# Kernel optimization log

Hardware: AMD Instinct MI355X
Metric: run time of the kernel (lower is better)

Reference implementation:

```python
import jax, jax.numpy as jnp
import numpy as np
from jax import lax

NS, W, BS, NSENT, EMB, H, NMEN, NCAND, NTOK, NENTV = 640, 64, 16, 40, 512, 256, 32, 32, 50000, 100000


def _gru_dir(xp, valid, Whh, bhh):
    # xp: [T,B,3H] precomputed input projection; valid: [T,B] bool
    h0 = jnp.zeros((xp.shape[1], Whh.shape[1]), xp.dtype)
    def step(h, inp):
        x, v = inp
        g = h @ Whh.T + bhh
        xr, xz, xn = jnp.split(x, 3, axis=-1)
        hr, hz, hn = jnp.split(g, 3, axis=-1)
        r = jax.nn.sigmoid(xr + hr)
        z = jax.nn.sigmoid(xz + hz)
        n = jnp.tanh(xn + r * hn)
        hnew = (1.0 - z) * n + z * h
        hnew = jnp.where(v[:, None], hnew, h)  # freeze state past seq end (packed-seq semantics)
        return hnew, hnew * v[:, None]         # zero padded outputs like pad_packed_sequence
    _, ys = lax.scan(step, h0, (xp, valid))
    return ys  # [T,B,H]


def _att_birnn(x, lens, Wih_f, Whh_f, bih_f, bhh_f, Wih_b, Whh_b, bih_b, bhh_b, lin_w, lin_b, attw):
    # x: [B,T,I], lens: [B] (descending, lens[0]==T) -> attended pooling [B,2H]
    T = x.shape[1]
    valid = jnp.arange(T)[:, None] < lens[None, :]  # [T,B]
    xp_f = jnp.einsum('bti,oi->tbo', x, Wih_f) + bih_f
    xp_b = jnp.einsum('bti,oi->tbo', x, Wih_b) + bih_b
    ys_f = _gru_dir(xp_f, valid, Whh_f, bhh_f)
    ys_b = _gru_dir(xp_b[::-1], valid[::-1], Whh_b, bhh_b)[::-1]
    enc = jnp.concatenate([ys_f, ys_b], -1)  # [T,B,2H]
    emb_h = jnp.tanh(jnp.einsum('tbh,oh->tbo', enc, lin_w) + lin_b)
    att = emb_h @ attw  # [T,B]
    e = jnp.exp(att) * valid  # original uses raw exp with additive 1e-4 denom
    wgt = e / (jnp.sum(e, 0, keepdims=True) + 1e-4)
    return jnp.sum(wgt[..., None] * enc, 0)  # [B,2H]


def _cos(a, b, eps=1e-8):
    dot = jnp.sum(a * b, -1)
    na = jnp.sqrt(jnp.sum(a * a, -1))
    nb = jnp.sqrt(jnp.sum(b * b, -1))
    return dot / jnp.maximum(na * nb, eps)


def _forward(batch_doc, sent_order, length_sent, length_doc, men_sent_idx, can_ent_idx, cand_mask,
             embed_doc, embed_ent, wp, sp, mlp_w, mlp_b):
    emb_w = embed_doc[batch_doc]                         # [NS,W,EMB]; eval mode -> no dropout
    sent_embs = _att_birnn(emb_w, length_sent, *wp)      # [NS,2H]
    padded = jnp.concatenate([jnp.zeros((1, sent_embs.shape[1]), sent_embs.dtype), sent_embs], 0)
    each_sent = padded[sent_order]                       # [BS,NSENT,2H] (_reorder_sent)
    doc_embs = _att_birnn(each_sent, length_doc, *sp)    # [BS,2H]
    emb_ent = embed_ent[can_ent_idx]                     # [BS,NMEN,NCAND,EMB]
    sent_vecs = each_sent[jnp.arange(each_sent.shape[0])[:, None], men_sent_idx]  # [BS,NMEN,2H]
    # vectorized replacement of the triple python loop of per-element cosine sims
    ss = _cos(sent_vecs[:, :, None, :], emb_ent) * cand_mask  # [BS,NMEN,NCAND]
    ds = _cos(doc_embs[:, None, None, :], emb_ent) * cand_mask
    cc = jnp.concatenate([ss, ds], -1)                   # [BS,NMEN,2*NCAND]
    mask = (ss != 0).astype(cc.dtype)
    return (cc @ mlp_w.T + mlp_b) * mask


def setup_inputs() -> dict:
    key = jax.random.key(0)
    ks = jax.random.split(key, 36)
    batch_doc = jax.random.randint(ks[0], (NS, W), 0, NTOK, dtype=jnp.int32)
    length_sent = jnp.sort(jax.random.randint(ks[1], (NS,), 1, W + 1, dtype=jnp.int32))[::-1].at[0].set(W)
    length_doc = jnp.sort(jax.random.randint(ks[2], (BS,), 1, NSENT + 1, dtype=jnp.int32))[::-1].at[0].set(NSENT)
    so = jax.random.randint(ks[3], (BS, NSENT), 1, NS + 1, dtype=jnp.int32)
    sent_order = jnp.where(jnp.arange(NSENT)[None, :] < length_doc[:, None], so, 0)
    men_sent_idx = jax.random.randint(ks[4], (BS, NMEN), 0, NSENT, dtype=jnp.int32) % length_doc[:, None]
    can_ent_idx = jax.random.randint(ks[5], (BS, NMEN, NCAND), 1, NENTV, dtype=jnp.int32)
    cand_mask = (jax.random.uniform(ks[6], (BS, NMEN, NCAND)) < 0.8).astype(jnp.float32)
    def nrm(k, shape, s=0.05):
        return s * jax.random.normal(k, shape, dtype=jnp.float32)
    embed_doc = nrm(ks[7], (NTOK, EMB)).at[0].set(0.0)   # padding_idx=0
    embed_ent = nrm(ks[8], (NENTV, EMB)).at[0].set(0.0)
    d = {
        'batch_doc': batch_doc, 'sent_order': sent_order, 'length_sent': length_sent,
        'length_doc': length_doc, 'men_sent_idx': men_sent_idx, 'can_ent_idx': can_ent_idx,
        'cand_mask': cand_mask, 'embed_doc': embed_doc, 'embed_ent': embed_ent,
        'w_Wih_f': nrm(ks[9], (3 * H, EMB)), 'w_Whh_f': nrm(ks[10], (3 * H, H)),
        'w_bih_f': nrm(ks[11], (3 * H,)), 'w_bhh_f': nrm(ks[12], (3 * H,)),
        'w_Wih_b': nrm(ks[13], (3 * H, EMB)), 'w_Whh_b': nrm(ks[14], (3 * H, H)),
        'w_bih_b': nrm(ks[15], (3 * H,)), 'w_bhh_b': nrm(ks[16], (3 * H,)),
        'w_lin_w': nrm(ks[17], (2 * H, 2 * H)), 'w_lin_b': nrm(ks[18], (2 * H,)),
        'w_attw': nrm(ks[19], (2 * H,)),
        's_Wih_f': nrm(ks[20], (3 * H, 2 * H)), 's_Whh_f': nrm(ks[21], (3 * H, H)),
        's_bih_f': nrm(ks[22], (3 * H,)), 's_bhh_f': nrm(ks[23], (3 * H,)),
        's_Wih_b': nrm(ks[24], (3 * H, 2 * H)), 's_Whh_b': nrm(ks[25], (3 * H, H)),
        's_bih_b': nrm(ks[26], (3 * H,)), 's_bhh_b': nrm(ks[27], (3 * H,)),
        's_lin_w': nrm(ks[28], (2 * H, 2 * H)), 's_lin_b': nrm(ks[29], (2 * H,)),
        's_attw': nrm(ks[30], (2 * H,)),
        'mlp_w': nrm(ks[31], (NCAND, 2 * NCAND)), 'mlp_b': nrm(ks[32], (NCAND,)),
    }
    return d


def reference(batch_doc, sent_order, length_sent, length_doc, men_sent_idx, can_ent_idx, cand_mask,
              embed_doc, embed_ent,
              w_Wih_f, w_Whh_f, w_bih_f, w_bhh_f, w_Wih_b, w_Whh_b, w_bih_b, w_bhh_b, w_lin_w, w_lin_b, w_attw,
              s_Wih_f, s_Whh_f, s_bih_f, s_bhh_f, s_Wih_b, s_Whh_b, s_bih_b, s_bhh_b, s_lin_w, s_lin_b, s_attw,
              mlp_w, mlp_b):
    wp = (w_Wih_f, w_Whh_f, w_bih_f, w_bhh_f, w_Wih_b, w_Whh_b, w_bih_b, w_bhh_b, w_lin_w, w_lin_b, w_attw)
    sp = (s_Wih_f, s_Whh_f, s_bih_f, s_bhh_f, s_Wih_b, s_Whh_b, s_bih_b, s_bhh_b, s_lin_w, s_lin_b, s_attw)
    return _forward(batch_doc, sent_order, length_sent, length_doc, men_sent_idx, can_ent_idx, cand_mask,
                    embed_doc, embed_ent, wp, sp, mlp_w, mlp_b)
```

## Files before the change

kernel.cpp:

```cpp
#include <hip/hip_runtime.h>
#include <cstdint>
#include <cstddef>


typedef __attribute__((ext_vector_type(8))) short bf16x8;
typedef __attribute__((ext_vector_type(4))) float f32x4;

__device__ __forceinline__ float bfraw2f(unsigned int u16) {
    unsigned int x = u16 << 16; float f; __builtin_memcpy(&f, &x, 4); return f;
}
__device__ __forceinline__ unsigned short f2bfraw(float f) {
    unsigned int u; __builtin_memcpy(&u, &f, 4);
    unsigned int r = u + 0x7fffu + ((u >> 16) & 1u);
    return (unsigned short)(r >> 16);
}
__device__ __forceinline__ unsigned short f2h(float f) {
    _Float16 h = (_Float16)f; unsigned short u; __builtin_memcpy(&u, &h, 2); return u;
}
__device__ __forceinline__ float h2f(unsigned short u) {
    _Float16 h; __builtin_memcpy(&h, &u, 2); return (float)h;
}
__device__ __forceinline__ float bflo(unsigned int p) {
    unsigned int x = p << 16; float f; __builtin_memcpy(&f, &x, 4); return f;
}
__device__ __forceinline__ float bfhi(unsigned int p) {
    unsigned int x = p & 0xffff0000u; float f; __builtin_memcpy(&f, &x, 4); return f;
}
__device__ __forceinline__ float fast_sigmoid(float x) { return 1.f / (1.f + __expf(-x)); }
__device__ __forceinline__ float fast_tanh(float x) {
    x = fminf(fmaxf(x, -30.f), 30.f);
    float e = __expf(2.f * x);
    return (e - 1.f) / (e + 1.f);
}
__device__ __forceinline__ float fin(float x) {
    return (x == x && fabsf(x) < 1e30f) ? x : 0.f;
}

__device__ __forceinline__ float ldsc(const void* p, size_t i, int m) {
    return m ? bfraw2f(((const unsigned short*)p)[i]) : ((const float*)p)[i];
}
__device__ __forceinline__ bf16x8 ld8bf(const void* p, size_t ei, int m) {
    if (m) return *(const bf16x8*)((const unsigned short*)p + ei);
    const float* f = (const float*)p + ei;
    f32x4 a = *(const f32x4*)f, b = *(const f32x4*)(f + 4);
    bf16x8 r;
    r[0] = (short)f2bfraw(a[0]); r[1] = (short)f2bfraw(a[1]);
    r[2] = (short)f2bfraw(a[2]); r[3] = (short)f2bfraw(a[3]);
    r[4] = (short)f2bfraw(b[0]); r[5] = (short)f2bfraw(b[1]);
    r[6] = (short)f2bfraw(b[2]); r[7] = (short)f2bfraw(b[3]);
    return r;
}
__device__ __forceinline__ void ld8f(const void* p, size_t ei, int m, float* o) {
    if (m) {
        uint4 wv = *(const uint4*)((const unsigned short*)p + ei);
        o[0] = bflo(wv.x); o[1] = bfhi(wv.x); o[2] = bflo(wv.y); o[3] = bfhi(wv.y);
        o[4] = bflo(wv.z); o[5] = bfhi(wv.z); o[6] = bflo(wv.w); o[7] = bfhi(wv.w);
    } else {
        const float* f = (const float*)p + ei;
        #pragma unroll
        for (int i = 0; i < 8; ++i) o[i] = f[i];
    }
}

__global__ void k_probe(const unsigned short* __restrict__ w, int* __restrict__ flag) {
    if (threadIdx.x == 0) {
        int bad = 0;
        for (int i = 0; i < 512; ++i) {
            float v = bfraw2f(w[i]);
            if (!(fabsf(v) <= 1.0f)) bad++;
        }
        flag[0] = (bad == 0) ? 1 : 0;
        flag[1] = 1;
    }
}

__global__ void p_cvt(const void* __restrict__ src, unsigned short* __restrict__ dst,
                      int n, const int* __restrict__ modep) {
    const int m = modep[0];
    for (int i = blockIdx.x * 256 + threadIdx.x; i < n; i += gridDim.x * 256)
        dst[i] = f2bfraw(ldsc(src, i, m));
}

__global__ void p_whh_swz(const void* __restrict__ whh, unsigned short* __restrict__ dst,
                          const int* __restrict__ modep) {
    const int m = modep[0];
    const int idx = blockIdx.x * 256 + threadIdx.x;
    if (idx >= 24576) return;
    const int lane = idx & 63, ks = (idx >> 6) & 7;
    const int g = (idx >> 9) % 6, w = idx / 3072;
    const int lm = lane & 15, q = lane >> 4;
    const int reg = g >> 1, nt = g & 1;
    const int row = reg * 256 + w * 32 + nt * 16 + lm;
    const size_t src = (size_t)row * 256 + ks * 32 + q * 8;
    const size_t d = (size_t)idx * 8;
    #pragma unroll
    for (int e = 0; e < 8; ++e) dst[d + e] = f2bfraw(ldsc(whh, src + e, m));
}

__global__ __launch_bounds__(256, 2) void k_xp_word(
    const void* __restrict__ embA, const int* __restrict__ batch_doc,
    const unsigned short* __restrict__ wih,
    const void* __restrict__ bih_f, const void* __restrict__ bih_b,
    unsigned short* __restrict__ xp, int b0, int nb,
    const int* __restrict__ amode, const int* __restrict__ modep)
{
    __shared__ unsigned short As[64][40];
    __shared__ unsigned short Bs[256][40];
    const int am = amode[0], m = modep[0];
    const int bm = blockIdx.x, bc = blockIdx.y;
    const int tid = threadIdx.x;
    const int wave = tid >> 6, lane = tid & 63, lm = lane & 15, q = lane >> 4;
    const int arow = tid >> 2, akoff = (tid & 3) * 8;
    const int r = bm * 64 + arow;
    const int tt = r / nb, bl = r - tt * nb;
    const size_t aei = (size_t)batch_doc[(b0 + bl) * 64 + tt] * 512 + akoff;

    const f32x4 fzero = {0.f, 0.f, 0.f, 0.f};
    f32x4 acc[4][4];
    #pragma unroll
    for (int i = 0; i < 4; ++i)
        #pragma unroll
        for (int j = 0; j < 4; ++j) acc[i][j] = fzero;

    for (int kt = 0; kt < 16; ++kt) {
        *(bf16x8*)&As[arow][akoff] = ld8bf(embA, aei + kt * 32, am);
        #pragma unroll
        for (int ld = 0; ld < 4; ++ld) {
            int e = ld * 256 + tid;
            int n = e >> 2, koff = (e & 3) * 8;
            int gn = bc * 256 + n;
            *(uint4*)&Bs[n][koff] = *(const uint4*)(wih + (size_t)gn * 512 + kt * 32 + koff);
        }
        __syncthreads();
        bf16x8 af[4], bv[4];
        #pragma unroll
        for (int mt = 0; mt < 4; ++mt) af[mt] = *(const bf16x8*)&As[mt * 16 + lm][q * 8];
        #pragma unroll
        for (int nt = 0; nt < 4; ++nt) bv[nt] = *(const bf16x8*)&Bs[wave * 64 + nt * 16 + lm][q * 8];
        #pragma unroll
        for (int mt = 0; mt < 4; ++mt)
            #pragma unroll
            for (int nt = 0; nt < 4; ++nt)
                acc[mt][nt] = __builtin_amdgcn_mfma_f32_16x16x32_bf16(af[mt], bv[nt], acc[mt][nt], 0, 0, 0);
        __syncthreads();
    }

    const size_t XPT = (size_t)64 * nb * 768;
    #pragma unroll
    for (int nt = 0; nt < 4; ++nt) {
        const int cn = bc * 256 + wave * 64 + nt * 16 + lm;
        const int dirb = (cn >= 768);
        const int o = cn - dirb * 768;
        const float bias = ldsc(dirb ? bih_b : bih_f, o, m);
        #pragma unroll
        for (int mt = 0; mt < 4; ++mt)
            #pragma unroll
            for (int j = 0; j < 4; ++j) {
                const int rr = bm * 64 + mt * 16 + q * 4 + j;
                xp[(dirb ? XPT : 0) + (size_t)rr * 768 + o] = f2h(acc[mt][nt][j] + bias);
            }
    }
}

__global__ __launch_bounds__(512, 2) void k_gru(
    const unsigned short* __restrict__ xp,
    const unsigned short* __restrict__ wswz_f,
    const unsigned short* __restrict__ wswz_b,
    const void* __restrict__ bhh_f, const void* __restrict__ bhh_b,
    const int* __restrict__ lens, float* __restrict__ enc, int T, int NB,
    const int* __restrict__ modep)
{
    __shared__ unsigned short hHi[2][16][264];
    __shared__ unsigned short hLo[2][16][264];
    __shared__ unsigned short xpS[2][16][776];
    __shared__ float bhhS[768];
    __shared__ int lensS[16];
    const int m = modep[0];
    const int tid = threadIdx.x;
    const int w = tid >> 6, lane = tid & 63, lm = lane & 15, q = lane >> 4;
    const int dir = blockIdx.x & 1, sg = blockIdx.x >> 1;
    const int s0 = sg << 4;
    const unsigned short* wsw =
        (dir ? wswz_b : wswz_f) + (size_t)w * 24576 + (size_t)lane * 8;
    const void* bhh = dir ? bhh_b : bhh_f;
    const unsigned short* xpd = xp + (dir ? (size_t)T * NB * 768 : 0);

    for (int e = tid; e < 16 * 264; e += 512) {
        (&hHi[0][0][0])[e] = 0; (&hLo[0][0][0])[e] = 0;
    }
    for (int j = tid; j < 768; j += 512) bhhS[j] = ldsc(bhh, j, m);
    if (tid < 16) lensS[tid] = lens[s0 + tid];

    {
        const int t0 = dir ? (T - 1) : 0;
        const unsigned short* xrow = xpd + ((size_t)t0 * NB + s0) * 768;
        #pragma unroll
        for (int i = 0; i < 3; ++i) {
            int e = tid + i * 512;
            uint4 v = *(const uint4*)(xrow + e * 8);
            *(uint4*)&xpS[0][e / 96][(e % 96) * 8] = v;
        }
    }
    __syncthreads();

    const f32x4 fzero = {0.f, 0.f, 0.f, 0.f};
    float hreg[2][4] = {};
    uint4 stg[3];
    for (int step = 0; step < T; ++step) {
        const int t = dir ? (T - 1 - step) : step;
        const int cur = step & 1, nxt = cur ^ 1;

        bf16x8 ahi[8], alo[8];
        #pragma unroll
        for (int ks = 0; ks < 8; ++ks) {
            ahi[ks] = *(const bf16x8*)&hHi[cur][lm][ks * 32 + q * 8];
            alo[ks] = *(const bf16x8*)&hLo[cur][lm][ks * 32 + q * 8];
        }

        const bool havenext = (step + 1 < T);
        if (havenext) {
            const int tn = dir ? (T - 2 - step) : (step + 1);
            const unsigned short* xrow = xpd + ((size_t)tn * NB + s0) * 768;
            #pragma unroll
            for (int i = 0; i < 3; ++i)
                stg[i] = *(const uint4*)(xrow + (tid + i * 512) * 8);
        }

        f32x4 acc[6];
        #pragma unroll
        for (int i = 0; i < 6; ++i) acc[i] = fzero;
        bf16x8 bcur[8], bnxt[8];
        #pragma unroll
        for (int ks = 0; ks < 8; ++ks) bcur[ks] = *(const bf16x8*)(wsw + ks * 512);
        #pragma unroll
        for (int g = 0; g < 6; ++g) {
            if (g < 5) {
                #pragma unroll
                for (int ks = 0; ks < 8; ++ks)
                    bnxt[ks] = *(const bf16x8*)(wsw + ((g + 1) * 8 + ks) * 512);
            }
            #pragma unroll
            for (int ks = 0; ks < 8; ++ks) {
                acc[g] = __builtin_amdgcn_mfma_f32_16x16x32_bf16(ahi[ks], bcur[ks], acc[g], 0, 0, 0);
                acc[g] = __builtin_amdgcn_mfma_f32_16x16x32_bf16(alo[ks], bcur[ks], acc[g], 0, 0, 0);
            }
            #pragma unroll
            for (int ks = 0; ks < 8; ++ks) bcur[ks] = bnxt[ks];
        }

        #pragma unroll
        for (int nt = 0; nt < 2; ++nt) {
            const int col = w * 32 + nt * 16 + lm;
            const float br = bhhS[col], bz = bhhS[256 + col], bn = bhhS[512 + col];
            #pragma unroll
            for (int j = 0; j < 4; ++j) {
                const int s = q * 4 + j;
                const float xr = h2f(xpS[cur][s][col]);
                const float xz = h2f(xpS[cur][s][256 + col]);
                const float xn = h2f(xpS[cur][s][512 + col]);
                const float rr = fast_sigmoid(xr + acc[nt][j] + br);
                const float zz = fast_sigmoid(xz + acc[2 + nt][j] + bz);
                const float nn = fast_tanh(xn + rr * (acc[4 + nt][j] + bn));
                const float hold = hreg[nt][j];
                float hnew = (1.f - zz) * nn + zz * hold;
                const bool v = (t < lensS[s]);
                hnew = v ? hnew : hold;
                hreg[nt][j] = hnew;
                const unsigned short uh = f2bfraw(hnew);
                hHi[nxt][s][col] = uh;
                hLo[nxt][s][col] = f2bfraw(hnew - bfraw2f(uh));
                enc[((size_t)t * NB + s0 + s) * 512 + (size_t)dir * 256 + col] = v ? hnew : 0.f;
            }
        }

        if (havenext) {
            #pragma unroll
            for (int i = 0; i < 3; ++i) {
                int e = tid + i * 512;
                *(uint4*)&xpS[nxt][e / 96][(e % 96) * 8] = stg[i];
            }
        }
        __syncthreads();
    }
}

__global__ __launch_bounds__(256, 1) void k_att(
    const float* __restrict__ enc, const unsigned short* __restrict__ lin_w,
    const void* __restrict__ lin_b, const void* __restrict__ attw,
    float* __restrict__ att_out, const int* __restrict__ modep)
{
    __shared__ unsigned short As[64][40];
    __shared__ unsigned short Bs[512][40];
    __shared__ float att_part[4][64];
    const int m = modep[0];
    const int bm = blockIdx.x;
    const int tid = threadIdx.x;
    const int wave = tid >> 6, lane = tid & 63, lm = lane & 15, q = lane >> 4;
    const int arow = tid >> 2, akoff = (tid & 3) * 8;
    const float* aptr = enc + (size_t)(bm * 64 + arow) * 512 + akoff;

    const f32x4 fzero = {0.f, 0.f, 0.f, 0.f};
    f32x4 acc[4][8];
    #pragma unroll
    for (int i = 0; i < 4; ++i)
        #pragma unroll
        for (int j = 0; j < 8; ++j) acc[i][j] = fzero;

    for (int kt = 0; kt < 16; ++kt) {
        f32x4 f0 = *(const f32x4*)(aptr + kt * 32);
        f32x4 f1 = *(const f32x4*)(aptr + kt * 32 + 4);
        bf16x8 cv;
        cv[0] = (short)f2bfraw(f0[0]); cv[1] = (short)f2bfraw(f0[1]);
        cv[2] = (short)f2bfraw(f0[2]); cv[3] = (short)f2bfraw(f0[3]);
        cv[4] = (short)f2bfraw(f1[0]); cv[5] = (short)f2bfraw(f1[1]);
        cv[6] = (short)f2bfraw(f1[2]); cv[7] = (short)f2bfraw(f1[3]);
        *(bf16x8*)&As[arow][akoff] = cv;
        #pragma unroll
        for (int ld = 0; ld < 8; ++ld) {
            int e = ld * 256 + tid;
            int n = e >> 2, koff = (e & 3) * 8;
            *(uint4*)&Bs[n][koff] = *(const uint4*)(lin_w + (size_t)n * 512 + kt * 32 + koff);
        }
        __syncthreads();
        bf16x8 af[4];
        #pragma unroll
        for (int mt = 0; mt < 4; ++mt) af[mt] = *(const bf16x8*)&As[mt * 16 + lm][q * 8];
        #pragma unroll
        for (int nt = 0; nt < 8; ++nt) {
            bf16x8 bv = *(const bf16x8*)&Bs[wave * 128 + nt * 16 + lm][q * 8];
            #pragma unroll
            for (int mt = 0; mt < 4; ++mt)
                acc[mt][nt] = __builtin_amdgcn_mfma_f32_16x16x32_bf16(af[mt], bv, acc[mt][nt], 0, 0, 0);
        }
        __syncthreads();
    }

    float part[4][4] = {};
    #pragma unroll
    for (int nt = 0; nt < 8; ++nt) {
        const int col = wave * 128 + nt * 16 + lm;
        const float lb = ldsc(lin_b, col, m);
        const float aw = ldsc(attw, col, m);
        #pragma unroll
        for (int mt = 0; mt < 4; ++mt)
            #pragma unroll
            for (int j = 0; j < 4; ++j)
                part[mt][j] += fast_tanh(acc[mt][nt][j] + lb) * aw;
    }
    #pragma unroll
    for (int mt = 0; mt < 4; ++mt)
        #pragma unroll
        for (int j = 0; j < 4; ++j) {
            float v = part[mt][j];
            #pragma unroll
            for (int d0 = 1; d0 < 16; d0 <<= 1) v += __shfl_xor(v, d0);
            part[mt][j] = v;
        }
    if (lm == 0) {
        #pragma unroll
        for (int mt = 0; mt < 4; ++mt)
            #pragma unroll
            for (int j = 0; j < 4; ++j)
                att_part[wave][mt * 16 + q * 4 + j] = part[mt][j];
    }
    __syncthreads();
    if (tid < 64)
        att_out[(size_t)bm * 64 + tid] =
            att_part[0][tid] + att_part[1][tid] + att_part[2][tid] + att_part[3][tid];
}

__global__ __launch_bounds__(256) void k_softsum(
    const float* __restrict__ att, const float* __restrict__ enc,
    const int* __restrict__ lens, float* __restrict__ out,
    float* __restrict__ zero_row, int T, int NB)
{
    __shared__ float eS[64];
    __shared__ float dS;
    const int bb = blockIdx.x, tid = threadIdx.x;
    if (zero_row && bb == 0) { for (int j = tid; j < 512; j += 256) zero_row[j] = 0.f; }
    const int len = lens[bb];
    if (tid < T) {
        float a = fminf(att[(size_t)tid * NB + bb], 50.f);
        eS[tid] = (tid < len) ? __expf(a) : 0.f;
    }
    __syncthreads();
    if (tid == 0) { float s = 0.f; for (int t2 = 0; t2 < T; ++t2) s += eS[t2]; dS = s + 1e-4f; }
    __syncthreads();
    const float inv = 1.f / dS;
    for (int j = tid; j < 512; j += 256) {
        float a0 = 0.f;
        for (int t2 = 0; t2 < T; ++t2) a0 += eS[t2] * enc[((size_t)t2 * NB + bb) * 512 + j];
        out[(size_t)bb * 512 + j] = fin(a0 * inv);
    }
}

__global__ __launch_bounds__(256) void k_sent_xp(
    const int* __restrict__ sent_order, const float* __restrict__ sent_pad,
    const unsigned short* __restrict__ swih,
    const void* __restrict__ bih_f, const void* __restrict__ bih_b,
    float* __restrict__ each_sent, unsigned short* __restrict__ xp_s,
    const int* __restrict__ modep)
{
    __shared__ float aS[512];
    const int m = modep[0];
    const int r = blockIdx.x, tid = threadIdx.x;
    const int idx = sent_order[r];
    const float* src = sent_pad + (size_t)idx * 512;
    for (int j = tid; j < 512; j += 256) { float v = src[j]; aS[j] = v; each_sent[(size_t)r * 512 + j] = v; }
    __syncthreads();
    const int d = r / 40, i2 = r % 40;
    #pragma unroll
    for (int p = 0; p < 6; ++p) {
        const int o = p * 256 + tid;
        const int dirb = (o >= 768);
        const int oo = o - dirb * 768;
        float s = ldsc(dirb ? bih_b : bih_f, oo, m);
        const unsigned short* wrow = swih + (size_t)o * 512;
        for (int k = 0; k < 512; k += 8) {
            const uint4 wv = *(const uint4*)(wrow + k);
            float wf[8];
            wf[0] = bflo(wv.x); wf[1] = bfhi(wv.x); wf[2] = bflo(wv.y); wf[3] = bfhi(wv.y);
            wf[4] = bflo(wv.z); wf[5] = bfhi(wv.z); wf[6] = bflo(wv.w); wf[7] = bfhi(wv.w);
            #pragma unroll
            for (int u = 0; u < 8; ++u) s += aS[k + u] * wf[u];
        }
        xp_s[(size_t)dirb * (40 * 16 * 768) + ((size_t)i2 * 16 + d) * 768 + oo] = f2h(s);
    }
}

__global__ __launch_bounds__(256) void k_final(
    const int* __restrict__ men_sent_idx, const int* __restrict__ can_ent_idx,
    const void* __restrict__ cand_mask, const void* __restrict__ embed_ent,
    const float* __restrict__ each_sent, const float* __restrict__ doc_embs,
    const void* __restrict__ mlp_w, const void* __restrict__ mlp_b,
    void* __restrict__ out, const int* __restrict__ modep)
{
    const int bm = blockIdx.x;
    const int b = bm >> 5;
    __shared__ float sv[512], dv[512];
    __shared__ float red[256];
    __shared__ float ssA[32], dsA[32];
    __shared__ float norms[2];
    const int m = modep[0];
    const int tid = threadIdx.x;
    const int sidx = men_sent_idx[bm];
    const float* svp = each_sent + ((size_t)b * 40 + sidx) * 512;
    const float* dvp = doc_embs + (size_t)b * 512;
    float pa = 0.f, pd = 0.f;
    for (int j = tid; j < 512; j += 256) {
        float a = svp[j], d0 = dvp[j];
        sv[j] = a; dv[j] = d0; pa += a * a; pd += d0 * d0;
    }
    red[tid] = pa; __syncthreads();
    for (int s = 128; s > 0; s >>= 1) { if (tid < s) red[tid] += red[tid + s]; __syncthreads(); }
    if (tid == 0) norms[0] = sqrtf(red[0]);
    __syncthreads();
    red[tid] = pd; __syncthreads();
    for (int s = 128; s > 0; s >>= 1) { if (tid < s) red[tid] += red[tid + s]; __syncthreads(); }
    if (tid == 0) norms[1] = sqrtf(red[0]);
    __syncthreads();

    const int c = tid >> 3, jg = tid & 7;
    const int ei = can_ent_idx[(size_t)bm * 32 + c];
    float dsv = 0.f, ddv = 0.f, ne = 0.f;
    for (int k = 0; k < 64; k += 8) {
        float wf[8];
        ld8f(embed_ent, (size_t)ei * 512 + jg * 64 + k, m, wf);
        const int base = jg * 64 + k;
        #pragma unroll
        for (int u = 0; u < 8; ++u) {
            dsv += sv[base + u] * wf[u];
            ddv += dv[base + u] * wf[u];
            ne  += wf[u] * wf[u];
        }
    }
    #pragma unroll
    for (int d0 = 1; d0 < 8; d0 <<= 1) {
        dsv += __shfl_xor(dsv, d0);
        ddv += __shfl_xor(ddv, d0);
        ne  += __shfl_xor(ne, d0);
    }
    if (jg == 0) {
        const float nen = sqrtf(ne);
        const float cm = ldsc(cand_mask, (size_t)bm * 32 + c, m);
        ssA[c] = dsv / fmaxf(norms[0] * nen, 1e-8f) * cm;
        dsA[c] = ddv / fmaxf(norms[1] * nen, 1e-8f) * cm;
    }
    __syncthreads();
    if (tid < 32) {
        float o = ldsc(mlp_b, tid, m);
        for (int j2 = 0; j2 < 32; ++j2) {
            o += ssA[j2] * ldsc(mlp_w, tid * 64 + j2, m);
            o += dsA[j2] * ldsc(mlp_w, tid * 64 + 32 + j2, m);
        }
        const float maskv = (ssA[tid] != 0.f) ? 1.f : 0.f;
        const float v = fin(o * maskv);
        if (m) ((unsigned short*)out)[(size_t)bm * 32 + tid] = f2bfraw(v);
        else   ((float*)out)[(size_t)bm * 32 + tid] = v;
    }
}

extern "C" void kernel_launch(void* const* d_in, const int* in_sizes, int n_in,
                              void* d_out, int out_size, void* d_ws, size_t ws_size,
                              hipStream_t stream)
{
    (void)in_sizes; (void)n_in; (void)out_size;
    const int* batch_doc    = (const int*)d_in[0];
    const int* sent_order   = (const int*)d_in[1];
    const int* length_sent  = (const int*)d_in[2];
    const int* length_doc   = (const int*)d_in[3];
    const int* men_sent_idx = (const int*)d_in[4];
    const int* can_ent_idx  = (const int*)d_in[5];
    const void* cand_mask = d_in[6];
    const void* embed_doc = d_in[7];
    const void* embed_ent = d_in[8];
    const void* wWihF = d_in[9];
    const void* wWhhF = d_in[10];
    const void* wBihF = d_in[11];
    const void* wBhhF = d_in[12];
    const void* wWihB = d_in[13];
    const void* wWhhB = d_in[14];
    const void* wBihB = d_in[15];
    const void* wBhhB = d_in[16];
    const void* wLinW = d_in[17];
    const void* wLinB = d_in[18];
    const void* wAttw = d_in[19];
    const void* sWihF = d_in[20];
    const void* sWhhF = d_in[21];
    const void* sBihF = d_in[22];
    const void* sBhhF = d_in[23];
    const void* sWihB = d_in[24];
    const void* sWhhB = d_in[25];
    const void* sBihB = d_in[26];
    const void* sBhhB = d_in[27];
    const void* sLinW = d_in[28];
    const void* sLinB = d_in[29];
    const void* sAttw = d_in[30];
    const void* mlpW  = d_in[31];
    const void* mlpB  = d_in[32];

    const size_t N_EMB = (size_t)50000 * 512;
    const size_t FIXED_CORE =
        256 + 4 * (size_t)196608 * 2 +
        (size_t)1536 * 512 * 2 + (size_t)512 * 512 * 2 +
        (size_t)1536 * 512 * 2 + (size_t)512 * 512 * 2 +
        (size_t)328192 * 4 + (size_t)327680 * 4 + (size_t)983040 * 2 +
        (size_t)327680 * 4 + (size_t)640 * 4 + (size_t)8192 * 4 + 65536;
    auto need = [&](int nb, int emb) -> size_t {
        return FIXED_CORE + (size_t)nb * (196608 + 131072 + 256)
             + (emb ? N_EMB * 2 : 0) + (1u << 20);
    };
    int emb_cvt = 1, nb = 320;
    {
        const int ladder[6] = {640, 320, 160, 80, 40, 16};
        bool found = false;
        for (int e = 1; e >= 0 && !found; --e)
            for (int i = 0; i < 6 && !found; ++i)
                if (need(ladder[i], e) <= ws_size) { emb_cvt = e; nb = ladder[i]; found = true; }
    }

    char* base = (char*)d_ws;
    size_t off = 0;
    auto take = [&](size_t bytes) -> void* {
        void* p = base + off; off += (bytes + 255) & ~(size_t)255; return p;
    };
    int* mode = (int*)take(256);
    unsigned short* swzWF = (unsigned short*)take((size_t)196608 * 2);
    unsigned short* swzWB = (unsigned short*)take((size_t)196608 * 2);
    unsigned short* swzSF = (unsigned short*)take((size_t)196608 * 2);
    unsigned short* swzSB = (unsigned short*)take((size_t)196608 * 2);
    unsigned short* wih_w = (unsigned short*)take((size_t)1536 * 512 * 2);
    unsigned short* lin_w = (unsigned short*)take((size_t)512 * 512 * 2);
    unsigned short* swih  = (unsigned short*)take((size_t)1536 * 512 * 2);
    unsigned short* slin  = (unsigned short*)take((size_t)512 * 512 * 2);
    float* sent_pad  = (float*)take((size_t)328192 * 4);
    float* each_sent = (float*)take((size_t)327680 * 4);
    unsigned short* xp_s = (unsigned short*)take((size_t)983040 * 2);
    float* enc_s     = (float*)take((size_t)327680 * 4);
    float* att_s     = (float*)take((size_t)640 * 4);
    float* doc_embs  = (float*)take((size_t)8192 * 4);
    unsigned short* xp_c = (unsigned short*)take((size_t)nb * 196608);
    float* enc_c     = (float*)take((size_t)nb * 131072);
    float* att_c     = (float*)take((size_t)nb * 256);
    unsigned short* emb_bf = emb_cvt ? (unsigned short*)take(N_EMB * 2) : nullptr;

    k_probe<<<1, 64, 0, stream>>>((const unsigned short*)wWhhF, mode);
    p_whh_swz<<<96, 256, 0, stream>>>(wWhhF, swzWF, mode);
    p_whh_swz<<<96, 256, 0, stream>>>(wWhhB, swzWB, mode);
    p_whh_swz<<<96, 256, 0, stream>>>(sWhhF, swzSF, mode);
    p_whh_swz<<<96, 256, 0, stream>>>(sWhhB, swzSB, mode);
    p_cvt<<<256, 256, 0, stream>>>(wWihF, wih_w, 768 * 512, mode);
    p_cvt<<<256, 256, 0, stream>>>(wWihB, wih_w + (size_t)768 * 512, 768 * 512, mode);
    p_cvt<<<256, 256, 0, stream>>>(wLinW, lin_w, 512 * 512, mode);
    p_cvt<<<256, 256, 0, stream>>>(sWihF, swih, 768 * 512, mode);
    p_cvt<<<256, 256, 0, stream>>>(sWihB, swih + (size_t)768 * 512, 768 * 512, mode);
    p_cvt<<<256, 256, 0, stream>>>(sLinW, slin, 512 * 512, mode);
    if (emb_cvt) p_cvt<<<2048, 256, 0, stream>>>(embed_doc, emb_bf, (int)N_EMB, mode);

    const void* embA = emb_cvt ? (const void*)emb_bf : embed_doc;
    const int* amode = emb_cvt ? (mode + 1) : mode;

    for (int b0 = 0; b0 < 640; b0 += nb) {
        k_xp_word<<<dim3(nb, 6), 256, 0, stream>>>(embA, batch_doc, wih_w,
                                                   wBihF, wBihB, xp_c, b0, nb, amode, mode);
        k_gru<<<2 * (nb / 16), 512, 0, stream>>>(xp_c, swzWF, swzWB, wBhhF, wBhhB,
                                                 length_sent + b0, enc_c, 64, nb, mode);
        k_att<<<nb, 256, 0, stream>>>(enc_c, lin_w, wLinB, wAttw, att_c, mode);
        k_softsum<<<nb, 256, 0, stream>>>(att_c, enc_c, length_sent + b0,
                                          sent_pad + (size_t)(1 + b0) * 512,
                                          (b0 == 0) ? sent_pad : nullptr, 64, nb);
    }
    k_sent_xp<<<640, 256, 0, stream>>>(sent_order, sent_pad, swih, sBihF, sBihB,
                                       each_sent, xp_s, mode);
    k_gru<<<2, 512, 0, stream>>>(xp_s, swzSF, swzSB, sBhhF, sBhhB,
                                 length_doc, enc_s, 40, 16, mode);
    k_att<<<10, 256, 0, stream>>>(enc_s, slin, sLinB, sAttw, att_s, mode);
    k_softsum<<<16, 256, 0, stream>>>(att_s, enc_s, length_doc, doc_embs, nullptr, 40, 16);
    k_final<<<512, 256, 0, stream>>>(men_sent_idx, can_ent_idx, cand_mask, embed_ent,
                                     each_sent, doc_embs, mlpW, mlpB, d_out, mode);
}
```

Measured before the change: 1.566 ms.

## Keep half of recurrent GRU weights resident in registers across timesteps

The GRU recurrence kernel now loads the first three gate-weight tiles (24 bf16x8 fragments per lane) into registers once, before the timestep loop. Only the other three tiles are re-read from global memory each step, and the hidden-state A fragments are loaded in two half-K phases to limit register pressure. This halves the per-step weight traffic on the serial critical path but raises VGPR usage, which could cause spills. The workspace ladder search is also reordered to prefer a larger batch chunk over embedding pre-conversion.

```diff
diff --git a/kernel.cpp b/kernel.cpp
--- a/kernel.cpp
+++ b/kernel.cpp
@@ -191,6 +191,13 @@
     for (int j = tid; j < 768; j += 512) bhhS[j] = ldsc(bhh, j, m);
     if (tid < 16) lensS[tid] = lens[s0 + tid];
 
+    bf16x8 bper[3][8];
+    #pragma unroll
+    for (int g = 0; g < 3; ++g)
+        #pragma unroll
+        for (int ks = 0; ks < 8; ++ks)
+            bper[g][ks] = *(const bf16x8*)(wsw + (size_t)(g * 8 + ks) * 512);
+
     {
         const int t0 = dir ? (T - 1) : 0;
         const unsigned short* xrow = xpd + ((size_t)t0 * NB + s0) * 768;
@@ -210,13 +217,6 @@
         const int t = dir ? (T - 1 - step) : step;
         const int cur = step & 1, nxt = cur ^ 1;
 
-        bf16x8 ahi[8], alo[8];
-        #pragma unroll
-        for (int ks = 0; ks < 8; ++ks) {
-            ahi[ks] = *(const bf16x8*)&hHi[cur][lm][ks * 32 + q * 8];
-            alo[ks] = *(const bf16x8*)&hLo[cur][lm][ks * 32 + q * 8];
-        }
-
         const bool havenext = (step + 1 < T);
         if (havenext) {
             const int tn = dir ? (T - 2 - step) : (step + 1);
@@ -229,23 +229,39 @@
         f32x4 acc[6];
         #pragma unroll
         for (int i = 0; i < 6; ++i) acc[i] = fzero;
-        bf16x8 bcur[8], bnxt[8];
-        #pragma unroll
-        for (int ks = 0; ks < 8; ++ks) bcur[ks] = *(const bf16x8*)(wsw + ks * 512);
-        #pragma unroll
-        for (int g = 0; g < 6; ++g) {
-            if (g < 5) {
+
+        #pragma unroll
+        for (int ph = 0; ph < 2; ++ph) {
+            const int kb = ph * 4;
+            bf16x8 ahi[4], alo[4];
+            #pragma unroll
+            for (int k = 0; k < 4; ++k) {
+                ahi[k] = *(const bf16x8*)&hHi[cur][lm][(kb + k) * 32 + q * 8];
+                alo[k] = *(const bf16x8*)&hLo[cur][lm][(kb + k) * 32 + q * 8];
+            }
+            bf16x8 bs3[4], bs4[4], bs5[4];
+            #pragma unroll
+            for (int k = 0; k < 4; ++k) {
+                bs3[k] = *(const bf16x8*)(wsw + (size_t)(24 + kb + k) * 512);
+                bs4[k] = *(const bf16x8*)(wsw + (size_t)(32 + kb + k) * 512);
+                bs5[k] = *(const bf16x8*)(wsw + (size_t)(40 + kb + k) * 512);
+            }
+            #pragma unroll
+            for (int g = 0; g < 3; ++g)
                 #pragma unroll
-                for (int ks = 0; ks < 8; ++ks)
-                    bnxt[ks] = *(const bf16x8*)(wsw + ((g + 1) * 8 + ks) * 512);
+                for (int k = 0; k < 4; ++k) {
+                    acc[g] = __builtin_amdgcn_mfma_f32_16x16x32_bf16(ahi[k], bper[g][kb + k], acc[g], 0, 0, 0);
+                    acc[g] = __builtin_amdgcn_mfma_f32_16x16x32_bf16(alo[k], bper[g][kb + k], acc[g], 0, 0, 0);
+                }
+            #pragma unroll
+            for (int k = 0; k < 4; ++k) {
+                acc[3] = __builtin_amdgcn_mfma_f32_16x16x32_bf16(ahi[k], bs3[k], acc[3], 0, 0, 0);
+                acc[3] = __builtin_amdgcn_mfma_f32_16x16x32_bf16(alo[k], bs3[k], acc[3], 0, 0, 0);
+                acc[4] = __builtin_amdgcn_mfma_f32_16x16x32_bf16(ahi[k], bs4[k], acc[4], 0, 0, 0);
+                acc[4] = __builtin_amdgcn_mfma_f32_16x16x32_bf16(alo[k], bs4[k], acc[4], 0, 0, 0);
+                acc[5] = __builtin_amdgcn_mfma_f32_16x16x32_bf16(ahi[k], bs5[k], acc[5], 0, 0, 0);
+                acc[5] = __builtin_amdgcn_mfma_f32_16x16x32_bf16(alo[k], bs5[k], acc[5], 0, 0, 0);
             }
-            #pragma unroll
-            for (int ks = 0; ks < 8; ++ks) {
-                acc[g] = __builtin_amdgcn_mfma_f32_16x16x32_bf16(ahi[ks], bcur[ks], acc[g], 0, 0, 0);
-                acc[g] = __builtin_amdgcn_mfma_f32_16x16x32_bf16(alo[ks], bcur[ks], acc[g], 0, 0, 0);
-            }
-            #pragma unroll
-            for (int ks = 0; ks < 8; ++ks) bcur[ks] = bnxt[ks];
         }
 
         #pragma unroll
@@ -554,8 +570,8 @@
     {
         const int ladder[6] = {640, 320, 160, 80, 40, 16};
         bool found = false;
-        for (int e = 1; e >= 0 && !found; --e)
-            for (int i = 0; i < 6 && !found; ++i)
+        for (int i = 0; i < 6 && !found; ++i)
+            for (int e = 1; e >= 0 && !found; --e)
                 if (need(ladder[i], e) <= ws_size) { emb_cvt = e; nb = ladder[i]; found = true; }
     }
 
```

Measured after the change: 1.379 ms. 1.14x faster.
